# Kernel optimization log

Hardware: AMD Instinct MI355X
Metric: run time of the kernel (lower is better)

Reference implementation:

```python
import jax, jax.numpy as jnp
import numpy as np

N_NODES = 50000
N_EDGES = 800000
HIDDEN = 128


def setup_inputs() -> dict:
    key = jax.random.key(0)
    k1, k2, k3, k4, k5 = jax.random.split(key, 5)
    x = jax.random.normal(k1, (N_NODES, HIDDEN), dtype=jnp.float32)
    src = jax.random.randint(k2, (N_EDGES,), 0, N_NODES, dtype=jnp.int32)
    # guarantee every node has in-degree >= 1 so deg**-0.5 is finite
    dst = jnp.concatenate([
        jnp.arange(N_NODES, dtype=jnp.int32),
        jax.random.randint(k3, (N_EDGES - N_NODES,), 0, N_NODES, dtype=jnp.int32),
    ])
    edge_index = jnp.stack([src, dst], axis=0)  # [2, E] (row0=j/src, row1=i/dst)
    # nn.Linear(hidden, hidden) params (reused twice in the original module)
    lim = 1.0 / np.sqrt(HIDDEN)
    W = jax.random.uniform(k4, (HIDDEN, HIDDEN), jnp.float32, -lim, lim)
    b = jax.random.uniform(k5, (HIDDEN,), jnp.float32, -lim, lim)
    return {"x": x, "W": W, "b": b, "edge_index": edge_index}


def reference(x, W, b, edge_index):
    src, dst = edge_index[0], edge_index[1]  # (j, i)
    n = x.shape[0]
    # in-degree via scatter-add
    deg = jnp.zeros((n,), x.dtype).at[dst].add(jnp.ones_like(dst, x.dtype))
    deg_inv_sqrt = deg ** -0.5
    norm = deg_inv_sqrt[src] * deg_inv_sqrt[dst]  # [E]
    # first linear (same weights used twice in original)
    h = x @ W.T + b  # [N, H]
    # COO SpMM: gather source rows, scale, scatter-add to destinations
    msg = h[src] * norm[:, None]  # [E, H]
    agg = jax.ops.segment_sum(msg, dst, num_segments=n)  # [N, H]
    # second linear + exact-erf GELU (torch default); dropout is identity in eval
    out = jax.nn.gelu(agg @ W.T + b, approximate=False)
    return out
```

## Files before the change

kernel.cpp:

```cpp
#include <hip/hip_runtime.h>
#include <hip/hip_bf16.h>

#define HIDDEN 128
#define CAP 64
#define BCAP 8192
#define CHUNK 1024

typedef __attribute__((ext_vector_type(8))) short bf16x8;
typedef __attribute__((ext_vector_type(4))) float f32x4;

__device__ __forceinline__ unsigned short f2bf(float f) {
    unsigned int u = __float_as_uint(f);
    u += 0x7FFFu + ((u >> 16) & 1u);
    return (unsigned short)(u >> 16);
}

__device__ __forceinline__ float bflo(unsigned int u) { return __uint_as_float(u << 16); }
__device__ __forceinline__ float bfhi(unsigned int u) { return __uint_as_float(u & 0xffff0000u); }

__global__ void prep_kernel(const float* __restrict__ x, const float* __restrict__ W,
                            unsigned short* __restrict__ xb, unsigned short* __restrict__ wb,
                            int nx4, int nw4, int partBlocks,
                            const int* __restrict__ ei, int E,
                            unsigned int* __restrict__ cursor,
                            unsigned int* __restrict__ lists,
                            int N) {
    __shared__ unsigned int hist[256], basea[256], cur[256];
    if ((int)blockIdx.x >= partBlocks) {
        int i = (blockIdx.x - partBlocks) * blockDim.x + threadIdx.x;
        if (i < nx4) {
            float4 v = ((const float4*)x)[i];
            ushort4 o;
            o.x = f2bf(v.x); o.y = f2bf(v.y); o.z = f2bf(v.z); o.w = f2bf(v.w);
            ((ushort4*)xb)[i] = o;
        } else {
            int j = i - nx4;
            if (j < nw4) {
                float4 v = ((const float4*)W)[j];
                ushort4 o;
                o.x = f2bf(v.x); o.y = f2bf(v.y); o.z = f2bf(v.z); o.w = f2bf(v.w);
                ((ushort4*)wb)[j] = o;
            }
        }
        return;
    }
    int e0 = blockIdx.x * CHUNK;
    int e1 = e0 + CHUNK; if (e1 > E) e1 = E;
    int tid = threadIdx.x;
    hist[tid] = 0;
    __syncthreads();
    for (int e = e0 + tid; e < e1; e += 256)
        atomicAdd(&hist[ei[E + e] >> 8], 1u);
    __syncthreads();
    unsigned int h = hist[tid];
    basea[tid] = h ? atomicAdd(&cursor[tid], h) : 0u;
    cur[tid] = 0;
    __syncthreads();
    for (int e = e0 + tid; e < e1; e += 256) {
        int s = ei[e];
        int d = ei[E + e];
        int bk = d >> 8;
        unsigned int pos = atomicAdd(&cur[bk], 1u) + basea[bk];
        if (pos < BCAP)
            lists[(size_t)bk * BCAP + pos] = ((unsigned int)s << 8) | (unsigned int)(d & 255);
    }
}

__global__ void buildcsr_kernel(const unsigned int* __restrict__ cursor,
                                const unsigned int* __restrict__ lists,
                                unsigned short* __restrict__ csr,
                                unsigned char* __restrict__ cnt_out,
                                float* __restrict__ dinv, int N) {
    __shared__ unsigned int lcnt[256];
    __shared__ unsigned short lcsr[256 * CAP];
    int b = blockIdx.x;
    int tid = threadIdx.x;
    lcnt[tid] = 0;
    __syncthreads();
    int count = (int)cursor[b]; if (count > BCAP) count = BCAP;
    for (int i = tid; i < count; i += 256) {
        unsigned int pk = lists[(size_t)b * BCAP + i];
        int local = pk & 255;
        unsigned int slot = atomicAdd(&lcnt[local], 1u);
        if (slot < CAP) lcsr[local * CAP + slot] = (unsigned short)(pk >> 8);
    }
    __syncthreads();
    int node = b * 256 + tid;
    if (node < N) {
        unsigned int deg = lcnt[tid];
        cnt_out[node] = (unsigned char)(deg > CAP ? CAP : deg);
        dinv[node] = deg ? rsqrtf((float)deg) : 0.0f;
    }
    const unsigned int* s32 = (const unsigned int*)lcsr;
    unsigned int* d32 = (unsigned int*)(csr + (size_t)b * 256 * CAP);
#pragma unroll
    for (int i = 0; i < 256 * CAP / 2 / 256; i++)
        d32[tid + i * 256] = s32[tid + i * 256];
}

__global__ void agg_kernel(const unsigned char* __restrict__ cnt,
                           const unsigned short* __restrict__ csr,
                           const float* __restrict__ dinv,
                           const unsigned short* __restrict__ xb,
                           unsigned short* __restrict__ yb, float* __restrict__ cvec, int n) {
    int lane = threadIdx.x & 63;
    int wid  = threadIdx.x >> 6;
    int gl   = lane & 15;
    int node = blockIdx.x * 16 + wid * 4 + (lane >> 4);
    if (node >= n) return;

    int deg = cnt[node];
    float di = dinv[node];
    const unsigned short* seg = csr + (size_t)node * CAP;

    float acc0 = 0, acc1 = 0, acc2 = 0, acc3 = 0, acc4 = 0, acc5 = 0, acc6 = 0, acc7 = 0;
    float fs = 0.0f;

    for (int be = 0; be < deg; be += 16) {
        int m = deg - be; if (m > 16) m = 16;
        int sv = (gl < m) ? (int)seg[be + gl] : 0;
        float dvv = (gl < m) ? dinv[sv] : 0.0f;
        for (int e = 0; e < m; e++) {
            int s = __shfl(sv, e, 16);
            float f = __shfl(dvv, e, 16) * di;
            fs += f;
            uint4 hv = *(const uint4*)(xb + (size_t)s * HIDDEN + gl * 8);
            acc0 += f * bflo(hv.x); acc1 += f * bfhi(hv.x);
            acc2 += f * bflo(hv.y); acc3 += f * bfhi(hv.y);
            acc4 += f * bflo(hv.z); acc5 += f * bfhi(hv.z);
            acc6 += f * bflo(hv.w); acc7 += f * bfhi(hv.w);
        }
    }

    uint4 o;
    o.x = (unsigned int)f2bf(acc0) | ((unsigned int)f2bf(acc1) << 16);
    o.y = (unsigned int)f2bf(acc2) | ((unsigned int)f2bf(acc3) << 16);
    o.z = (unsigned int)f2bf(acc4) | ((unsigned int)f2bf(acc5) << 16);
    o.w = (unsigned int)f2bf(acc6) | ((unsigned int)f2bf(acc7) << 16);
    *(uint4*)(yb + (size_t)node * HIDDEN + gl * 8) = o;
    if (gl == 0) cvec[node] = fs;
}

__global__ void dgemm_kernel(const unsigned short* __restrict__ yb,
                             const unsigned short* __restrict__ wb,
                             const float* __restrict__ bias,
                             const float* __restrict__ cvec,
                             float* __restrict__ out, int nrows) {
    __shared__ unsigned short wlds[HIDDEN * HIDDEN];
    __shared__ unsigned short zs[4][16][136];
    int lane = threadIdx.x & 63;
    int wave = threadIdx.x >> 6;
    int base = blockIdx.x * 64 + wave * 16;
    int hi = lane >> 4, lo = lane & 15;

    for (int ci = threadIdx.x; ci < 1024; ci += 256) {
        int r = ci >> 3, c32 = ci & 7;
        const uint4* src = (const uint4*)(wb + (size_t)r * HIDDEN + c32 * 16);
        uint4 v0 = src[0], v1 = src[1];
        int b0 = r * 256 + c32 * 32;
        int sw = (r & 7) << 4;
        *(uint4*)((char*)wlds + (b0 ^ sw)) = v0;
        *(uint4*)((char*)wlds + ((b0 + 16) ^ sw)) = v1;
    }

    int arow = base + lo;
    if (arow >= nrows) arow = nrows - 1;
    const bf16x8* Ap = (const bf16x8*)(yb + (size_t)arow * HIDDEN + hi * 8);
    bf16x8 a0 = Ap[0], a1 = Ap[4], a2 = Ap[8], a3 = Ap[12];
    __syncthreads();

#define BFRAG(T, KK) \
    (*(const bf16x8*)((const char*)wlds + \
        ((((T) * 16 + lo) * 256 + (KK) * 64 + hi * 16) ^ ((lo & 7) << 4))))

    f32x4 acc[8];
#pragma unroll
    for (int t = 0; t < 8; t++) acc[t] = (f32x4)(0.0f);
#pragma unroll
    for (int t = 0; t < 8; t++) {
        acc[t] = __builtin_amdgcn_mfma_f32_16x16x32_bf16(a0, BFRAG(t, 0), acc[t], 0, 0, 0);
        acc[t] = __builtin_amdgcn_mfma_f32_16x16x32_bf16(a1, BFRAG(t, 1), acc[t], 0, 0, 0);
        acc[t] = __builtin_amdgcn_mfma_f32_16x16x32_bf16(a2, BFRAG(t, 2), acc[t], 0, 0, 0);
        acc[t] = __builtin_amdgcn_mfma_f32_16x16x32_bf16(a3, BFRAG(t, 3), acc[t], 0, 0, 0);
    }

    float cv[4];
#pragma unroll
    for (int i = 0; i < 4; i++) {
        int r = base + hi * 4 + i;
        cv[i] = cvec[r < nrows ? r : nrows - 1];
    }
#pragma unroll
    for (int t = 0; t < 8; t++) {
        float bv = bias[t * 16 + lo];
#pragma unroll
        for (int i = 0; i < 4; i++)
            zs[wave][hi * 4 + i][t * 16 + lo] = f2bf(acc[t][i] + cv[i] * bv);
    }

    bf16x8 z0 = *(const bf16x8*)&zs[wave][lo][0 * 32 + hi * 8];
    bf16x8 z1 = *(const bf16x8*)&zs[wave][lo][1 * 32 + hi * 8];
    bf16x8 z2 = *(const bf16x8*)&zs[wave][lo][2 * 32 + hi * 8];
    bf16x8 z3 = *(const bf16x8*)&zs[wave][lo][3 * 32 + hi * 8];

    f32x4 acc2[8];
#pragma unroll
    for (int t = 0; t < 8; t++) acc2[t] = (f32x4)(0.0f);
#pragma unroll
    for (int t = 0; t < 8; t++) {
        acc2[t] = __builtin_amdgcn_mfma_f32_16x16x32_bf16(z0, BFRAG(t, 0), acc2[t], 0, 0, 0);
        acc2[t] = __builtin_amdgcn_mfma_f32_16x16x32_bf16(z1, BFRAG(t, 1), acc2[t], 0, 0, 0);
        acc2[t] = __builtin_amdgcn_mfma_f32_16x16x32_bf16(z2, BFRAG(t, 2), acc2[t], 0, 0, 0);
        acc2[t] = __builtin_amdgcn_mfma_f32_16x16x32_bf16(z3, BFRAG(t, 3), acc2[t], 0, 0, 0);
    }
#undef BFRAG

#pragma unroll
    for (int t = 0; t < 8; t++) {
        int col = t * 16 + lo;
        float bv = bias[col];
#pragma unroll
        for (int i = 0; i < 4; i++) {
            int r = base + hi * 4 + i;
            if (r < nrows) {
                float v = acc2[t][i] + bv;
                v = 0.5f * v * (1.0f + erff(v * 0.70710678118f));
                out[(size_t)r * HIDDEN + col] = v;
            }
        }
    }
}

extern "C" void kernel_launch(void* const* d_in, const int* in_sizes, int n_in,
                              void* d_out, int out_size, void* d_ws, size_t ws_size,
                              hipStream_t stream) {
    const float* x  = (const float*)d_in[0];
    const float* W  = (const float*)d_in[1];
    const float* b  = (const float*)d_in[2];
    const int*   ei = (const int*)d_in[3];

    int N = in_sizes[0] / HIDDEN;
    int E = in_sizes[3] / 2;
    int NB = (N + 255) >> 8;

    char* ws = (char*)d_ws;
    size_t off = 0;
    unsigned int* cursor = (unsigned int*)(ws + off);    off += 1024;
    unsigned int* lists = (unsigned int*)(ws + off);     off += (((size_t)NB * BCAP * 4) + 255) & ~255ull;
    unsigned short* csr = (unsigned short*)(ws + off);   off += (((size_t)NB * 256 * CAP * 2) + 255) & ~255ull;
    unsigned char* cnt = (unsigned char*)(ws + off);     off += (((size_t)N) + 255) & ~255ull;
    float* dinv = (float*)(ws + off);                    off += (((size_t)N * 4) + 255) & ~255ull;
    unsigned short* xb = (unsigned short*)(ws + off);    off += (((size_t)N * HIDDEN * 2) + 255) & ~255ull;
    unsigned short* wb = (unsigned short*)(ws + off);    off += ((HIDDEN * HIDDEN * 2) + 255) & ~255ull;
    unsigned short* yb = (unsigned short*)(ws + off);    off += (((size_t)N * HIDDEN * 2) + 255) & ~255ull;
    float* cvec = (float*)(ws + off);                    off += (((size_t)N * 4) + 255) & ~255ull;

    hipMemsetAsync(cursor, 0, 1024, stream);

    int nx4 = N * HIDDEN / 4, nw4 = HIDDEN * HIDDEN / 4;
    int convBlocks = (nx4 + nw4 + 255) / 256;
    int partBlocks = (E + CHUNK - 1) / CHUNK;
    prep_kernel<<<partBlocks + convBlocks, 256, 0, stream>>>(
        x, W, xb, wb, nx4, nw4, partBlocks, ei, E, cursor, lists, N);
    buildcsr_kernel<<<NB, 256, 0, stream>>>(cursor, lists, csr, cnt, dinv, N);
    agg_kernel<<<(N + 15) / 16, 256, 0, stream>>>(cnt, csr, dinv, xb, yb, cvec, N);
    dgemm_kernel<<<(N + 63) / 64, 256, 0, stream>>>(yb, wb, b, cvec, (float*)d_out, N);
}
```

Baseline: 167.8 us.

## Precompose W·W into single matrix, drop cursor memset, widen CSR build blocks

Precomputes M = W·W (bf16) and b2 = W·b in an extra block of the CSR-build kernel, so the final kernel does one MFMA GEMM with the composed matrix instead of two chained GEMMs through LDS. The cursor array moves to a device global that the CSR builder resets after reading, which removes the hipMemsetAsync launch. CSR build blocks grow to 512 threads. The composed matrix is rounded to bf16, which changes numerics slightly, and the cursor reset relies on the first call starting from zero-initialised globals.

```diff
diff --git a/kernel.cpp b/kernel.cpp
--- a/kernel.cpp
+++ b/kernel.cpp
@@ -9,6 +9,8 @@
 typedef __attribute__((ext_vector_type(8))) short bf16x8;
 typedef __attribute__((ext_vector_type(4))) float f32x4;
 
+__device__ unsigned int g_cursor[256];
+
 __device__ __forceinline__ unsigned short f2bf(float f) {
     unsigned int u = __float_as_uint(f);
     u += 0x7FFFu + ((u >> 16) & 1u);
@@ -22,9 +24,7 @@
                             unsigned short* __restrict__ xb, unsigned short* __restrict__ wb,
                             int nx4, int nw4, int partBlocks,
                             const int* __restrict__ ei, int E,
-                            unsigned int* __restrict__ cursor,
-                            unsigned int* __restrict__ lists,
-                            int N) {
+                            unsigned int* __restrict__ lists) {
     __shared__ unsigned int hist[256], basea[256], cur[256];
     if ((int)blockIdx.x >= partBlocks) {
         int i = (blockIdx.x - partBlocks) * blockDim.x + threadIdx.x;
@@ -53,7 +53,7 @@
         atomicAdd(&hist[ei[E + e] >> 8], 1u);
     __syncthreads();
     unsigned int h = hist[tid];
-    basea[tid] = h ? atomicAdd(&cursor[tid], h) : 0u;
+    basea[tid] = h ? atomicAdd(&g_cursor[tid], h) : 0u;
     cur[tid] = 0;
     __syncthreads();
     for (int e = e0 + tid; e < e1; e += 256) {
@@ -66,36 +66,94 @@
     }
 }
 
-__global__ void buildcsr_kernel(const unsigned int* __restrict__ cursor,
-                                const unsigned int* __restrict__ lists,
+__global__ void buildcsr_kernel(const unsigned int* __restrict__ lists,
                                 unsigned short* __restrict__ csr,
                                 unsigned char* __restrict__ cnt_out,
-                                float* __restrict__ dinv, int N) {
-    __shared__ unsigned int lcnt[256];
-    __shared__ unsigned short lcsr[256 * CAP];
+                                float* __restrict__ dinv, int N, int NB,
+                                const unsigned short* __restrict__ wb,
+                                const float* __restrict__ Wf,
+                                const float* __restrict__ bf,
+                                unsigned short* __restrict__ mb,
+                                float* __restrict__ b2) {
+    __shared__ unsigned char smem[34816];
     int b = blockIdx.x;
     int tid = threadIdx.x;
-    lcnt[tid] = 0;
-    __syncthreads();
-    int count = (int)cursor[b]; if (count > BCAP) count = BCAP;
-    for (int i = tid; i < count; i += 256) {
-        unsigned int pk = lists[(size_t)b * BCAP + i];
-        int local = pk & 255;
-        unsigned int slot = atomicAdd(&lcnt[local], 1u);
-        if (slot < CAP) lcsr[local * CAP + slot] = (unsigned short)(pk >> 8);
-    }
-    __syncthreads();
-    int node = b * 256 + tid;
-    if (node < N) {
-        unsigned int deg = lcnt[tid];
-        cnt_out[node] = (unsigned char)(deg > CAP ? CAP : deg);
-        dinv[node] = deg ? rsqrtf((float)deg) : 0.0f;
-    }
-    const unsigned int* s32 = (const unsigned int*)lcsr;
-    unsigned int* d32 = (unsigned int*)(csr + (size_t)b * 256 * CAP);
-#pragma unroll
-    for (int i = 0; i < 256 * CAP / 2 / 256; i++)
-        d32[tid + i * 256] = s32[tid + i * 256];
+    if (b < NB) {
+        unsigned int* lcnt = (unsigned int*)smem;
+        unsigned short* lcsr = (unsigned short*)(smem + 1024);
+        __shared__ int scount;
+        if (tid < 256) lcnt[tid] = 0;
+        if (tid == 0) {
+            int c = (int)g_cursor[b];
+            scount = c > BCAP ? BCAP : c;
+            g_cursor[b] = 0;
+        }
+        __syncthreads();
+        int count = scount;
+        const unsigned int* lp = lists + (size_t)b * BCAP;
+        for (int i = tid; i < count; i += 512) {
+            unsigned int pk = lp[i];
+            int local = pk & 255;
+            unsigned int slot = atomicAdd(&lcnt[local], 1u);
+            if (slot < CAP) lcsr[local * CAP + slot] = (unsigned short)(pk >> 8);
+        }
+        __syncthreads();
+        int node = b * 256 + tid;
+        if (tid < 256 && node < N) {
+            unsigned int deg = lcnt[tid];
+            cnt_out[node] = (unsigned char)(deg > CAP ? CAP : deg);
+            dinv[node] = deg ? rsqrtf((float)deg) : 0.0f;
+        }
+        const unsigned int* s32 = (const unsigned int*)lcsr;
+        unsigned int* d32 = (unsigned int*)(csr + (size_t)b * 256 * CAP);
+#pragma unroll
+        for (int i = 0; i < 256 * CAP / 2 / 512; i++)
+            d32[tid + i * 512] = s32[tid + i * 512];
+        return;
+    }
+    unsigned short* wT = (unsigned short*)smem;
+#define WT_ADDR(K, Jb) ((((K) * 272 + (Jb)) ^ ((((K) >> 3) & 7) << 4)))
+    for (int i = tid; i < 2048; i += 512) {
+        int j = i >> 4, kq = i & 15;
+        uint4 v = ((const uint4*)wb)[i];
+        unsigned short e[8];
+        e[0] = (unsigned short)v.x; e[1] = (unsigned short)(v.x >> 16);
+        e[2] = (unsigned short)v.y; e[3] = (unsigned short)(v.y >> 16);
+        e[4] = (unsigned short)v.z; e[5] = (unsigned short)(v.z >> 16);
+        e[6] = (unsigned short)v.w; e[7] = (unsigned short)(v.w >> 16);
+#pragma unroll
+        for (int u = 0; u < 8; u++)
+            *(unsigned short*)((char*)wT + WT_ADDR(kq * 8 + u, j * 2)) = e[u];
+    }
+    __syncthreads();
+    int lane = tid & 63, wave = tid >> 6;
+    int hi = lane >> 4, lo = lane & 15;
+    int base = wave * 16;
+    const bf16x8* Ap = (const bf16x8*)(wb + (size_t)(base + lo) * HIDDEN + hi * 8);
+    bf16x8 a0 = Ap[0], a1 = Ap[4], a2 = Ap[8], a3 = Ap[12];
+    f32x4 acc[8];
+#pragma unroll
+    for (int t = 0; t < 8; t++) acc[t] = (f32x4)(0.0f);
+#pragma unroll
+    for (int t = 0; t < 8; t++) {
+#define WTFRAG(T, KK) (*(const bf16x8*)((char*)wT + WT_ADDR((T) * 16 + lo, ((KK) * 32 + hi * 8) * 2)))
+        acc[t] = __builtin_amdgcn_mfma_f32_16x16x32_bf16(a0, WTFRAG(t, 0), acc[t], 0, 0, 0);
+        acc[t] = __builtin_amdgcn_mfma_f32_16x16x32_bf16(a1, WTFRAG(t, 1), acc[t], 0, 0, 0);
+        acc[t] = __builtin_amdgcn_mfma_f32_16x16x32_bf16(a2, WTFRAG(t, 2), acc[t], 0, 0, 0);
+        acc[t] = __builtin_amdgcn_mfma_f32_16x16x32_bf16(a3, WTFRAG(t, 3), acc[t], 0, 0, 0);
+#undef WTFRAG
+    }
+#pragma unroll
+    for (int t = 0; t < 8; t++)
+#pragma unroll
+        for (int i = 0; i < 4; i++)
+            mb[(size_t)(base + hi * 4 + i) * HIDDEN + t * 16 + lo] = f2bf(acc[t][i]);
+    if (tid < 128) {
+        float s = 0.0f;
+        for (int k = 0; k < 128; k++) s += Wf[tid * 128 + k] * bf[k];
+        b2[tid] = s;
+    }
+#undef WT_ADDR
 }
 
 __global__ void agg_kernel(const unsigned char* __restrict__ cnt,
@@ -113,7 +171,7 @@
     float di = dinv[node];
     const unsigned short* seg = csr + (size_t)node * CAP;
 
-    float acc0 = 0, acc1 = 0, acc2 = 0, acc3 = 0, acc4 = 0, acc5 = 0, acc6 = 0, acc7 = 0;
+    float a0 = 0, a1 = 0, a2 = 0, a3 = 0, a4 = 0, a5 = 0, a6 = 0, a7 = 0;
     float fs = 0.0f;
 
     for (int be = 0; be < deg; be += 16) {
@@ -125,29 +183,29 @@
             float f = __shfl(dvv, e, 16) * di;
             fs += f;
             uint4 hv = *(const uint4*)(xb + (size_t)s * HIDDEN + gl * 8);
-            acc0 += f * bflo(hv.x); acc1 += f * bfhi(hv.x);
-            acc2 += f * bflo(hv.y); acc3 += f * bfhi(hv.y);
-            acc4 += f * bflo(hv.z); acc5 += f * bfhi(hv.z);
-            acc6 += f * bflo(hv.w); acc7 += f * bfhi(hv.w);
+            a0 += f * bflo(hv.x); a1 += f * bfhi(hv.x);
+            a2 += f * bflo(hv.y); a3 += f * bfhi(hv.y);
+            a4 += f * bflo(hv.z); a5 += f * bfhi(hv.z);
+            a6 += f * bflo(hv.w); a7 += f * bfhi(hv.w);
         }
     }
 
     uint4 o;
-    o.x = (unsigned int)f2bf(acc0) | ((unsigned int)f2bf(acc1) << 16);
-    o.y = (unsigned int)f2bf(acc2) | ((unsigned int)f2bf(acc3) << 16);
-    o.z = (unsigned int)f2bf(acc4) | ((unsigned int)f2bf(acc5) << 16);
-    o.w = (unsigned int)f2bf(acc6) | ((unsigned int)f2bf(acc7) << 16);
+    o.x = (unsigned int)f2bf(a0) | ((unsigned int)f2bf(a1) << 16);
+    o.y = (unsigned int)f2bf(a2) | ((unsigned int)f2bf(a3) << 16);
+    o.z = (unsigned int)f2bf(a4) | ((unsigned int)f2bf(a5) << 16);
+    o.w = (unsigned int)f2bf(a6) | ((unsigned int)f2bf(a7) << 16);
     *(uint4*)(yb + (size_t)node * HIDDEN + gl * 8) = o;
     if (gl == 0) cvec[node] = fs;
 }
 
-__global__ void dgemm_kernel(const unsigned short* __restrict__ yb,
-                             const unsigned short* __restrict__ wb,
+__global__ void gemm2_kernel(const unsigned short* __restrict__ yb,
+                             const unsigned short* __restrict__ mb,
                              const float* __restrict__ bias,
+                             const float* __restrict__ b2,
                              const float* __restrict__ cvec,
                              float* __restrict__ out, int nrows) {
-    __shared__ unsigned short wlds[HIDDEN * HIDDEN];
-    __shared__ unsigned short zs[4][16][136];
+    __shared__ unsigned short mlds[HIDDEN * HIDDEN];
     int lane = threadIdx.x & 63;
     int wave = threadIdx.x >> 6;
     int base = blockIdx.x * 64 + wave * 16;
@@ -155,12 +213,12 @@
 
     for (int ci = threadIdx.x; ci < 1024; ci += 256) {
         int r = ci >> 3, c32 = ci & 7;
-        const uint4* src = (const uint4*)(wb + (size_t)r * HIDDEN + c32 * 16);
+        const uint4* src = (const uint4*)(mb + (size_t)r * HIDDEN + c32 * 16);
         uint4 v0 = src[0], v1 = src[1];
         int b0 = r * 256 + c32 * 32;
         int sw = (r & 7) << 4;
-        *(uint4*)((char*)wlds + (b0 ^ sw)) = v0;
-        *(uint4*)((char*)wlds + ((b0 + 16) ^ sw)) = v1;
+        *(uint4*)((char*)mlds + (b0 ^ sw)) = v0;
+        *(uint4*)((char*)mlds + ((b0 + 16) ^ sw)) = v1;
     }
 
     int arow = base + lo;
@@ -170,7 +228,7 @@
     __syncthreads();
 
 #define BFRAG(T, KK) \
-    (*(const bf16x8*)((const char*)wlds + \
+    (*(const bf16x8*)((const char*)mlds + \
         ((((T) * 16 + lo) * 256 + (KK) * 64 + hi * 16) ^ ((lo & 7) << 4))))
 
     f32x4 acc[8];
@@ -183,6 +241,7 @@
         acc[t] = __builtin_amdgcn_mfma_f32_16x16x32_bf16(a2, BFRAG(t, 2), acc[t], 0, 0, 0);
         acc[t] = __builtin_amdgcn_mfma_f32_16x16x32_bf16(a3, BFRAG(t, 3), acc[t], 0, 0, 0);
     }
+#undef BFRAG
 
     float cv[4];
 #pragma unroll
@@ -192,38 +251,13 @@
     }
 #pragma unroll
     for (int t = 0; t < 8; t++) {
-        float bv = bias[t * 16 + lo];
-#pragma unroll
-        for (int i = 0; i < 4; i++)
-            zs[wave][hi * 4 + i][t * 16 + lo] = f2bf(acc[t][i] + cv[i] * bv);
-    }
-
-    bf16x8 z0 = *(const bf16x8*)&zs[wave][lo][0 * 32 + hi * 8];
-    bf16x8 z1 = *(const bf16x8*)&zs[wave][lo][1 * 32 + hi * 8];
-    bf16x8 z2 = *(const bf16x8*)&zs[wave][lo][2 * 32 + hi * 8];
-    bf16x8 z3 = *(const bf16x8*)&zs[wave][lo][3 * 32 + hi * 8];
-
-    f32x4 acc2[8];
-#pragma unroll
-    for (int t = 0; t < 8; t++) acc2[t] = (f32x4)(0.0f);
-#pragma unroll
-    for (int t = 0; t < 8; t++) {
-        acc2[t] = __builtin_amdgcn_mfma_f32_16x16x32_bf16(z0, BFRAG(t, 0), acc2[t], 0, 0, 0);
-        acc2[t] = __builtin_amdgcn_mfma_f32_16x16x32_bf16(z1, BFRAG(t, 1), acc2[t], 0, 0, 0);
-        acc2[t] = __builtin_amdgcn_mfma_f32_16x16x32_bf16(z2, BFRAG(t, 2), acc2[t], 0, 0, 0);
-        acc2[t] = __builtin_amdgcn_mfma_f32_16x16x32_bf16(z3, BFRAG(t, 3), acc2[t], 0, 0, 0);
-    }
-#undef BFRAG
-
-#pragma unroll
-    for (int t = 0; t < 8; t++) {
         int col = t * 16 + lo;
-        float bv = bias[col];
+        float bv = bias[col], b2v = b2[col];
 #pragma unroll
         for (int i = 0; i < 4; i++) {
             int r = base + hi * 4 + i;
             if (r < nrows) {
-                float v = acc2[t][i] + bv;
+                float v = acc[t][i] + cv[i] * b2v + bv;
                 v = 0.5f * v * (1.0f + erff(v * 0.70710678118f));
                 out[(size_t)r * HIDDEN + col] = v;
             }
@@ -242,27 +276,27 @@
     int N = in_sizes[0] / HIDDEN;
     int E = in_sizes[3] / 2;
     int NB = (N + 255) >> 8;
+    int partBlocks = (E + CHUNK - 1) / CHUNK;
 
     char* ws = (char*)d_ws;
     size_t off = 0;
-    unsigned int* cursor = (unsigned int*)(ws + off);    off += 1024;
-    unsigned int* lists = (unsigned int*)(ws + off);     off += (((size_t)NB * BCAP * 4) + 255) & ~255ull;
-    unsigned short* csr = (unsigned short*)(ws + off);   off += (((size_t)NB * 256 * CAP * 2) + 255) & ~255ull;
-    unsigned char* cnt = (unsigned char*)(ws + off);     off += (((size_t)N) + 255) & ~255ull;
-    float* dinv = (float*)(ws + off);                    off += (((size_t)N * 4) + 255) & ~255ull;
-    unsigned short* xb = (unsigned short*)(ws + off);    off += (((size_t)N * HIDDEN * 2) + 255) & ~255ull;
-    unsigned short* wb = (unsigned short*)(ws + off);    off += ((HIDDEN * HIDDEN * 2) + 255) & ~255ull;
-    unsigned short* yb = (unsigned short*)(ws + off);    off += (((size_t)N * HIDDEN * 2) + 255) & ~255ull;
-    float* cvec = (float*)(ws + off);                    off += (((size_t)N * 4) + 255) & ~255ull;
-
-    hipMemsetAsync(cursor, 0, 1024, stream);
+    unsigned int* lists = (unsigned int*)(ws + off);    off += (((size_t)NB * BCAP * 4) + 255) & ~255ull;
+    unsigned short* csr = (unsigned short*)(ws + off);  off += (((size_t)NB * 256 * CAP * 2) + 255) & ~255ull;
+    unsigned char* cnt = (unsigned char*)(ws + off);    off += (((size_t)NB * 256) + 255) & ~255ull;
+    float* dinv = (float*)(ws + off);                   off += (((size_t)N * 4) + 255) & ~255ull;
+    unsigned short* xb = (unsigned short*)(ws + off);   off += (((size_t)N * HIDDEN * 2) + 255) & ~255ull;
+    unsigned short* wb = (unsigned short*)(ws + off);   off += ((HIDDEN * HIDDEN * 2) + 255) & ~255ull;
+    unsigned short* mb = (unsigned short*)(ws + off);   off += ((HIDDEN * HIDDEN * 2) + 255) & ~255ull;
+    float* b2 = (float*)(ws + off);                     off += ((HIDDEN * 4) + 255) & ~255ull;
+    unsigned short* yb = (unsigned short*)(ws + off);   off += (((size_t)N * HIDDEN * 2) + 255) & ~255ull;
+    float* cvec = (float*)(ws + off);                   off += (((size_t)N * 4) + 255) & ~255ull;
 
     int nx4 = N * HIDDEN / 4, nw4 = HIDDEN * HIDDEN / 4;
     int convBlocks = (nx4 + nw4 + 255) / 256;
-    int partBlocks = (E + CHUNK - 1) / CHUNK;
     prep_kernel<<<partBlocks + convBlocks, 256, 0, stream>>>(
-        x, W, xb, wb, nx4, nw4, partBlocks, ei, E, cursor, lists, N);
-    buildcsr_kernel<<<NB, 256, 0, stream>>>(cursor, lists, csr, cnt, dinv, N);
+        x, W, xb, wb, nx4, nw4, partBlocks, ei, E, lists);
+    buildcsr_kernel<<<NB + 1, 512, 0, stream>>>(lists, csr, cnt, dinv, N, NB,
+                                                wb, W, b, mb, b2);
     agg_kernel<<<(N + 15) / 16, 256, 0, stream>>>(cnt, csr, dinv, xb, yb, cvec, N);
-    dgemm_kernel<<<(N + 63) / 64, 256, 0, stream>>>(yb, wb, b, cvec, (float*)d_out, N);
-}
+    gemm2_kernel<<<(N + 63) / 64, 256, 0, stream>>>(yb, mb, b, b2, cvec, (float*)d_out, N);
+}
```

New measurement: 162.4 us. 3.3% less time.
